# Kernel tuning notes

Hardware: AMD Instinct MI355X
Metric: run time of the kernel (lower is better)

Reference implementation:

```python
import jax, jax.numpy as jnp
import numpy as np

NUM_HEAD = 16
NUM_SEQ = 2048
NUM_FEAT = 1024
HEAD_DIM = NUM_FEAT // NUM_HEAD
LN_EPS = 1e-5


def _constants():
    # decay per head: log(1 - 2^{-5-h})
    decay = jnp.log(1.0 - 2.0 ** (-5.0 - jnp.arange(NUM_HEAD, dtype=jnp.float32)))
    idx = jnp.arange(NUM_SEQ, dtype=jnp.float32)
    diff = idx[:, None] - idx[None, :]                      # [s, s]
    # exp(diff * decay) on lower triangle (incl. diagonal), 0 above
    mask = jnp.where(diff[None] >= 0, jnp.exp(diff[None] * decay[:, None, None]), 0.0)  # [h, s, s]
    # rotary angles: each frequency repeated twice
    angle = 1.0 / 10000.0 ** jnp.linspace(0.0, 1.0, HEAD_DIM // 2)
    angle = jnp.repeat(angle, 2)                            # [hd]
    sin = jnp.sin(idx[:, None] * angle[None, :])            # [s, hd]
    cos = jnp.cos(idx[:, None] * angle[None, :])
    return mask, sin, cos


def _rotate_every_two(x):
    x1 = x[..., ::2]
    x2 = x[..., 1::2]
    return jnp.stack((-x2, x1), axis=-1).reshape(x.shape)


def setup_inputs() -> dict:
    key = jax.random.key(0)
    ks = jax.random.split(key, 5)
    b, s, d = 4, NUM_SEQ, NUM_FEAT
    x = jax.random.normal(ks[0], (b, s, d), dtype=jnp.float32)
    Wq = jax.random.normal(ks[1], (d, d), dtype=jnp.float32) * 0.02
    Wk = jax.random.normal(ks[2], (d, d), dtype=jnp.float32) * 0.02
    Wv = jax.random.normal(ks[3], (d, d), dtype=jnp.float32) * 0.02
    Wo = jax.random.normal(ks[4], (d, d), dtype=jnp.float32) * 0.02
    ln_w = jnp.ones((HEAD_DIM,), dtype=jnp.float32)
    ln_b = jnp.zeros((HEAD_DIM,), dtype=jnp.float32)
    return {"x": x, "Wq": Wq, "Wk": Wk, "Wv": Wv, "Wo": Wo, "ln_w": ln_w, "ln_b": ln_b}


def reference(x, Wq, Wk, Wv, Wo, ln_w, ln_b):
    b, s, d = x.shape
    h, hd = NUM_HEAD, HEAD_DIM
    mask, sin, cos = _constants()

    def proj(W):
        # torch Linear (no bias): x @ W.T -> [b, h, s, hd]
        return (x @ W.T).reshape(b, s, h, hd).transpose(0, 2, 1, 3)

    q, k, v = proj(Wq), proj(Wk), proj(Wv)
    # rotary theta shift (sin/cos broadcast over batch & head)
    q = q * cos + _rotate_every_two(q) * sin
    k = k * cos + _rotate_every_two(k) * sin

    r = jnp.einsum('bhsd,bhtd->bhst', q, k) * mask[None]    # decay-masked scores
    o = jnp.einsum('bhst,bhtd->bhsd', r, v)                 # [b, h, s, hd]

    # LayerNorm over head_dim
    mu = jnp.mean(o, axis=-1, keepdims=True)
    var = jnp.var(o, axis=-1, keepdims=True)
    y = (o - mu) * jax.lax.rsqrt(var + LN_EPS) * ln_w + ln_b

    y = y.transpose(0, 2, 1, 3).reshape(b, s, d)
    return jax.nn.silu(y) @ Wo.T
```

## Files before the change

### kernel.cpp

```cpp
#include <hip/hip_runtime.h>
#include <math.h>

typedef unsigned short u16;
typedef __attribute__((ext_vector_type(8))) short short8;
typedef __attribute__((ext_vector_type(4))) float floatx4;

#define LDS_AS(p) ((__attribute__((address_space(3))) void*)(p))
#define GLB_AS(p) ((const __attribute__((address_space(1))) void*)(p))

__device__ __forceinline__ u16 f2bf(float f) {
  unsigned int u = __float_as_uint(f);
  u += 0x7fffu + ((u >> 16) & 1u);
  return (u16)(u >> 16);
}

__device__ __forceinline__ void gld16(const void* g, void* l) {
  __builtin_amdgcn_global_load_lds(GLB_AS(g), LDS_AS(l), 16, 0, 0);
}

__device__ __forceinline__ floatx4 mfma16(short8 a, short8 b, floatx4 c) {
  return __builtin_amdgcn_mfma_f32_16x16x32_bf16(a, b, c, 0, 0, 0);
}

__global__ void prep_kernel(const float* __restrict__ x, const float* __restrict__ Wq,
                            const float* __restrict__ Wk, const float* __restrict__ Wv,
                            const float* __restrict__ Wo, u16* __restrict__ xp,
                            u16* __restrict__ wqkvp, u16* __restrict__ wop,
                            float2* __restrict__ rtab) {
  int i = blockIdx.x * blockDim.x + threadIdx.x;
  const int str = gridDim.x * blockDim.x;
  for (; i < 3211264; i += str) {
    if (i < 3145728) {
      int U; u16* d;
      const float* s;
      if (i < 2097152)      { U = i;           d = xp;    s = x;  }
      else if (i < 2883584) { U = i - 2097152; d = wqkvp; s = nullptr; }
      else                  { U = i - 2883584; d = wop;   s = Wo; }
      const int tile = U >> 12;
      const int kc   = (U >> 7) & 31;
      const int lane = (U >> 1) & 63;
      const int jh   = U & 1;
      const int scol = kc * 32 + (lane >> 4) * 8 + jh * 4;
      int srow = tile * 16 + (lane & 15);
      if (s == nullptr) {
        const int sel = srow >> 10;
        srow &= 1023;
        s = (sel == 0) ? Wq : (sel == 1) ? Wk : Wv;
      }
      float4 v = ((const float4*)s)[srow * 256 + (scol >> 2)];
      ushort4 o;
      o.x = f2bf(v.x); o.y = f2bf(v.y); o.z = f2bf(v.z); o.w = f2bf(v.w);
      ((ushort4*)d)[U] = o;
    } else {
      const int t = i - 3145728;
      const int seq = t >> 5, dh = t & 31;
      const float freq = exp2f(-(float)dh * 0.42863594770f);
      float sn, cs;
      __sincosf((float)seq * freq, &sn, &cs);
      rtab[t] = make_float2(sn, cs);
    }
  }
}

template <int EPI>
__global__ __launch_bounds__(512, 4)
void gemm_bt(const u16* __restrict__ A, const u16* __restrict__ Bw, int K,
             u16* __restrict__ qb, u16* __restrict__ kb, u16* __restrict__ vtb,
             u16* __restrict__ kwt, const float2* __restrict__ rtab,
             float* __restrict__ outp) {
  __shared__ __align__(16) u16 smem[36864];
  const int tid = threadIdx.x;
  const int w = tid >> 6, lane = tid & 63;
  const int quad = lane >> 4, l15 = lane & 15;
  const int wr = w >> 2, wc = w & 3;
  const int m0 = blockIdx.y * 128, n0 = blockIdx.x * 256;

  const size_t tsz = (size_t)(K >> 5) * 512;
  const u16* Apk = A + ((size_t)(m0 >> 4) + w) * tsz + lane * 8;
  const u16* B0  = Bw + ((size_t)(n0 >> 4) + 2 * w) * tsz + lane * 8;
  const u16* B1  = B0 + tsz;

  auto stage = [&](int buf, int kc) {
    const int nb = buf * 12288;
    gld16(Apk + (size_t)kc * 512, &smem[nb + w * 512]);
    gld16(B0 + (size_t)kc * 512, &smem[nb + 4096 + (2 * w) * 512]);
    gld16(B1 + (size_t)kc * 512, &smem[nb + 4096 + (2 * w + 1) * 512]);
  };

  floatx4 acc[4][4] = {};
  const int NT = K >> 5;

  stage(0, 0);
  stage(1, 1);

  int cur = 0, stg = 2;
  for (int t = 0; t < NT; ++t) {
    if (t + 1 < NT)
      asm volatile("s_waitcnt vmcnt(3)" ::: "memory");
    else
      asm volatile("s_waitcnt vmcnt(0)" ::: "memory");
    __builtin_amdgcn_s_barrier();
    asm volatile("" ::: "memory");
    __builtin_amdgcn_sched_barrier(0);

    if (t + 2 < NT) stage(stg, t + 2);

    const u16* Ap = &smem[cur * 12288];
    const u16* Bp = &smem[cur * 12288 + 4096];
    short8 a[4], b[4];
#pragma unroll
    for (int i = 0; i < 4; ++i)
      a[i] = *(const short8*)&Ap[(wr * 4 + i) * 512 + lane * 8];
#pragma unroll
    for (int j = 0; j < 4; ++j)
      b[j] = *(const short8*)&Bp[(wc * 4 + j) * 512 + lane * 8];
    __builtin_amdgcn_s_setprio(1);
#pragma unroll
    for (int i = 0; i < 4; ++i)
#pragma unroll
      for (int j = 0; j < 4; ++j)
        acc[i][j] = mfma16(a[i], b[j], acc[i][j]);
    __builtin_amdgcn_s_setprio(0);
    asm volatile("" ::: "memory");
    cur = (cur == 2) ? 0 : cur + 1;
    stg = (stg == 2) ? 0 : stg + 1;
  }
  __builtin_amdgcn_s_barrier();

  u16* scr = &smem[w * 4096];

  const int mrb = m0 + wr * 64;
  const int ncb = n0 + wc * 64;

  if (EPI == 0) {
    const int which = n0 >> 10;
    const int c1024 = ncb & 1023;
    const int bidx = mrb >> 11;
    const int hh = c1024 >> 6;
    const int seq0 = mrb & 2047;
    const int lr = lane >> 3, lc = lane & 7;

    if (which < 2) {
#pragma unroll
      for (int j = 0; j < 4; ++j) {
        const int d = j * 16 + l15;
        const int dc = d >> 3, dl = d & 7;
#pragma unroll
        for (int i = 0; i < 4; ++i)
#pragma unroll
          for (int r = 0; r < 4; ++r) {
            const int sl = i * 16 + quad * 4 + r;
            const int seq = seq0 + sl;
            const float v = acc[i][j][r];
            const float p = __shfl_xor(v, 1, 64);
            const float2 sc = rtab[(d >> 1) + seq * 32];
            const float res = (d & 1) ? (v * sc.y + p * sc.x) : (v * sc.y - p * sc.x);
            scr[sl * 64 + (((dc + (sl >> 2)) & 7) << 3) + dl] = f2bf(res);
          }
      }
      u16* dst = ((which == 0) ? qb : kb) + (size_t)(bidx * 16 + hh) * 131072 +
                 (size_t)seq0 * 64;
#pragma unroll
      for (int cch = 0; cch < 8; ++cch) {
        const int row = cch * 8 + lr;
        const int slot = (lc + (row >> 2)) & 7;
        short8 vv = *(const short8*)&scr[row * 64 + slot * 8];
        *(short8*)(dst + (size_t)row * 64 + lc * 8) = vv;
      }
      if (which == 1) {
        const float l2h = __log2f(1.0f - exp2f(-(float)(5 + hh)));
#pragma unroll
        for (int j = 0; j < 4; ++j) {
          const int d = j * 16 + l15;
#pragma unroll
          for (int i = 0; i < 4; ++i) {
            ushort4 pk;
#pragma unroll
            for (int r = 0; r < 4; ++r) {
              const int sl = i * 16 + quad * 4 + r;
              const int seq = seq0 + sl;
              const float v = acc[i][j][r];
              const float p = __shfl_xor(v, 1, 64);
              const float2 sc = rtab[(d >> 1) + seq * 32];
              const float res = (d & 1) ? (v * sc.y + p * sc.x) : (v * sc.y - p * sc.x);
              const float wgt = exp2f((float)(127 - (seq & 127)) * l2h);
              ((u16*)&pk)[r] = f2bf(res * wgt);
            }
            *(ushort4*)&scr[d * 64 + ((i * 16 + quad * 4 + 8 * (d & 7)) & 63)] = pk;
          }
        }
        u16* dw = kwt + (size_t)(bidx * 16 + hh) * 131072 + seq0;
#pragma unroll
        for (int cch = 0; cch < 8; ++cch) {
          const int drow = cch * 8 + lr;
          const int slot = (lc + (drow & 7)) & 7;
          short8 vv = *(const short8*)&scr[drow * 64 + slot * 8];
          *(short8*)(dw + (size_t)drow * 2048 + lc * 8) = vv;
        }
      }
    } else {
#pragma unroll
      for (int j = 0; j < 4; ++j) {
        const int d = j * 16 + l15;
#pragma unroll
        for (int i = 0; i < 4; ++i) {
          ushort4 pk;
          pk.x = f2bf(acc[i][j][0]);
          pk.y = f2bf(acc[i][j][1]);
          pk.z = f2bf(acc[i][j][2]);
          pk.w = f2bf(acc[i][j][3]);
          *(ushort4*)&scr[d * 64 + ((i * 16 + quad * 4 + 8 * (d & 7)) & 63)] = pk;
        }
      }
      u16* dh = vtb + (size_t)(bidx * 16 + hh) * 131072 + seq0;
#pragma unroll
      for (int cch = 0; cch < 8; ++cch) {
        const int drow = cch * 8 + lr;
        const int slot = (lc + (drow & 7)) & 7;
        short8 vv = *(const short8*)&scr[drow * 64 + slot * 8];
        *(short8*)(dh + (size_t)drow * 2048 + lc * 8) = vv;
      }
    }
  } else {
    float* scrf = (float*)scr;
    const int lr4 = lane >> 4, lc16 = lane & 15;
#pragma unroll
    for (int p = 0; p < 4; ++p) {
#pragma unroll
      for (int j = 0; j < 4; ++j)
#pragma unroll
        for (int r = 0; r < 4; ++r)
          scrf[(quad * 4 + r) * 65 + j * 16 + l15] = acc[p][j][r];
#pragma unroll
      for (int cch = 0; cch < 4; ++cch) {
        const int rr = cch * 4 + lr4;
        float4 vv = *(const float4*)&scrf[rr * 65 + lc16 * 4];
        *(float4*)&outp[(size_t)(mrb + p * 16 + rr) * 1024 + ncb + lc16 * 4] = vv;
      }
    }
  }
}

__global__ __launch_bounds__(256, 4)
void kvchunk_kernel(const u16* __restrict__ kwt, const u16* __restrict__ vtb,
                    float* __restrict__ U) {
  __shared__ __align__(16) u16 kls[16 * 512];
  __shared__ __align__(16) u16 vls[16 * 512];
  const int c = blockIdx.x, bh = blockIdx.y;
  const int tid = threadIdx.x, w = tid >> 6, lane = tid & 63;
  const int quad = lane >> 4, l15 = lane & 15;
  const u16* kg = kwt + (size_t)bh * 131072 + c * 128;
  const u16* vg = vtb + (size_t)bh * 131072 + c * 128;
#pragma unroll
  for (int rg = 0; rg < 4; ++rg) {
    const int rid = w * 4 + rg;
    const int m = rid >> 2, kst = rid & 3;
    gld16(kg + (size_t)(m * 16 + l15) * 2048 + kst * 32 + quad * 8, &kls[rid * 512]);
    gld16(vg + (size_t)(m * 16 + l15) * 2048 + kst * 32 + quad * 8, &vls[rid * 512]);
  }
  __syncthreads();
  floatx4 acc[4] = {};
#pragma unroll
  for (int kst = 0; kst < 4; ++kst) {
    short8 bf = *(const short8*)&vls[(w * 4 + kst) * 512 + lane * 8];
#pragma unroll
    for (int m = 0; m < 4; ++m) {
      short8 af = *(const short8*)&kls[(m * 4 + kst) * 512 + lane * 8];
      acc[m] = mfma16(af, bf, acc[m]);
    }
  }
  float* Ub = U + ((size_t)bh * 16 + c) * 4096;
#pragma unroll
  for (int m = 0; m < 4; ++m)
#pragma unroll
    for (int r = 0; r < 4; ++r)
      Ub[(m * 16 + quad * 4 + r) * 64 + w * 16 + l15] = acc[m][r];
}

__global__ void scan_kernel(const float* __restrict__ U, u16* __restrict__ Sb) {
  const int bh = blockIdx.x;
  const int w = threadIdx.x >> 6, l = threadIdx.x & 63;
  const int h = bh & 15;
  const float l2 = __log2f(1.0f - exp2f(-(float)(5 + h)));
  const float lamL = exp2f(128.0f * l2);
  float S[16];
#pragma unroll
  for (int i = 0; i < 16; ++i) S[i] = 0.f;
  for (int c = 0; c < 16; ++c) {
    u16* sp = Sb + ((size_t)bh * 16 + c) * 4096 + l * 64 + w * 16;
#pragma unroll
    for (int dk = 0; dk < 16; dk += 4) {
      ushort4 pk;
      pk.x = f2bf(S[dk]);     pk.y = f2bf(S[dk + 1]);
      pk.z = f2bf(S[dk + 2]); pk.w = f2bf(S[dk + 3]);
      *(ushort4*)&sp[dk] = pk;
    }
    const float* up = U + ((size_t)bh * 16 + c) * 4096 + (w * 16) * 64 + l;
#pragma unroll
    for (int dk = 0; dk < 16; ++dk)
      S[dk] = lamL * S[dk] + up[dk * 64];
  }
}

__global__ __launch_bounds__(256, 2)
void attn_chunk_kernel(const u16* __restrict__ qb, const u16* __restrict__ kb,
                       const u16* __restrict__ vtb, const u16* __restrict__ Sb,
                       const float* __restrict__ lnw, const float* __restrict__ lnb,
                       u16* __restrict__ yb) {
  __shared__ __align__(16) u16 kls[16 * 512];
  __shared__ __align__(16) u16 vls[16 * 512];
  __shared__ __align__(16) u16 Sls[8 * 512];
  __shared__ __align__(16) u16 pls[4 * 32 * 40];

  const int c = blockIdx.x, bh = blockIdx.y, h = bh & 15;
  const int tid = threadIdx.x;
  const int w = tid >> 6, lane = tid & 63, quad = lane >> 4, l15 = lane & 15;
  const float l2 = __log2f(1.0f - exp2f(-(float)(5 + h)));

  const u16* kg = kb + (size_t)bh * 131072 + (size_t)c * 128 * 64;
  const u16* vg = vtb + (size_t)bh * 131072 + (size_t)c * 128;
  const u16* Sg = Sb + ((size_t)bh * 16 + c) * 4096;
#pragma unroll
  for (int rg = 0; rg < 4; ++rg) {
    const int kid = w * 4 + rg;
    const int nsub = kid >> 1, kk = kid & 1;
    gld16(kg + (size_t)(nsub * 16 + l15) * 64 + kk * 32 + quad * 8, &kls[kid * 512]);
    const int jd = kid >> 2, kst = kid & 3;
    gld16(vg + (size_t)(jd * 16 + l15) * 2048 + kst * 32 + quad * 8, &vls[kid * 512]);
  }
#pragma unroll
  for (int e = 0; e < 2; ++e) {
    const int rid = w * 2 + e;
    const int nd = rid >> 1, kk = rid & 1;
    gld16(Sg + (size_t)(nd * 16 + l15) * 64 + kk * 32 + quad * 8, &Sls[rid * 512]);
  }

  short8 qf[2][2];
  {
    const u16* qbase = qb + ((size_t)bh * 2048 + c * 128 + w * 32 + l15) * 64 + quad * 8;
#pragma unroll
    for (int i = 0; i < 2; ++i)
#pragma unroll
      for (int kk = 0; kk < 2; ++kk)
        qf[i][kk] = *(const short8*)(qbase + (size_t)i * 16 * 64 + kk * 32);
  }
  float lnwv[4], lnbv[4];
#pragma unroll
  for (int jd = 0; jd < 4; ++jd) {
    lnwv[jd] = lnw[jd * 16 + l15];
    lnbv[jd] = lnb[jd * 16 + l15];
  }
  __syncthreads();

  floatx4 sacc[2][8] = {};
#pragma unroll
  for (int kk = 0; kk < 2; ++kk) {
    short8 bf[8];
#pragma unroll
    for (int j = 0; j < 8; ++j)
      bf[j] = *(const short8*)&kls[(j * 2 + kk) * 512 + lane * 8];
#pragma unroll
    for (int i = 0; i < 2; ++i)
#pragma unroll
      for (int j = 0; j < 8; ++j)
        sacc[i][j] = mfma16(qf[i][kk], bf[j], sacc[i][j]);
  }

  floatx4 oacc[2][4] = {};
#pragma unroll
  for (int kk = 0; kk < 2; ++kk)
#pragma unroll
    for (int nd = 0; nd < 4; ++nd) {
      short8 sf = *(const short8*)&Sls[(nd * 2 + kk) * 512 + lane * 8];
#pragma unroll
      for (int i = 0; i < 2; ++i)
        oacc[i][nd] = mfma16(qf[i][kk], sf, oacc[i][nd]);
    }
  float rowf[8];
#pragma unroll
  for (int i = 0; i < 2; ++i)
#pragma unroll
    for (int r = 0; r < 4; ++r)
      rowf[i * 4 + r] = exp2f((float)(w * 32 + i * 16 + quad * 4 + r) * l2);
  const float lam1 = exp2f(l2);
#pragma unroll
  for (int i = 0; i < 2; ++i)
#pragma unroll
    for (int nd = 0; nd < 4; ++nd)
#pragma unroll
      for (int r = 0; r < 4; ++r)
        oacc[i][nd][r] *= rowf[i * 4 + r] * lam1;

  float colf[8];
#pragma unroll
  for (int j = 0; j < 8; ++j) colf[j] = exp2f(-(float)(j * 16 + l15) * l2);
  u16* pw = &pls[w * 1280];
#pragma unroll
  for (int kst = 0; kst < 4; ++kst) {
#pragma unroll
    for (int jl = 0; jl < 2; ++jl) {
      const int j = kst * 2 + jl;
#pragma unroll
      for (int i = 0; i < 2; ++i)
#pragma unroll
        for (int r = 0; r < 4; ++r) {
          const int srow = i * 16 + quad * 4 + r;
          const int dlt = (w * 32 + srow) - (j * 16 + l15);
          const float v =
              (dlt >= 0) ? sacc[i][j][r] * rowf[i * 4 + r] * colf[j] : 0.0f;
          pw[srow * 40 + jl * 16 + l15] = f2bf(v);
        }
    }
    short8 pf[2], vf[4];
#pragma unroll
    for (int i = 0; i < 2; ++i)
      pf[i] = *(const short8*)&pw[(i * 16 + l15) * 40 + quad * 8];
#pragma unroll
    for (int jd = 0; jd < 4; ++jd)
      vf[jd] = *(const short8*)&vls[(jd * 4 + kst) * 512 + lane * 8];
#pragma unroll
    for (int i = 0; i < 2; ++i)
#pragma unroll
      for (int jd = 0; jd < 4; ++jd)
        oacc[i][jd] = mfma16(pf[i], vf[jd], oacc[i][jd]);
  }

  __syncthreads();
  u16* scrw = &kls[w * 2048];
  const int b = bh >> 4;
#pragma unroll
  for (int i = 0; i < 2; ++i)
#pragma unroll
    for (int r = 0; r < 4; ++r) {
      float sum = 0.f, ssq = 0.f;
#pragma unroll
      for (int jd = 0; jd < 4; ++jd) {
        const float v = oacc[i][jd][r];
        sum += v;
        ssq += v * v;
      }
#pragma unroll
      for (int off = 1; off < 16; off <<= 1) {
        sum += __shfl_xor(sum, off, 64);
        ssq += __shfl_xor(ssq, off, 64);
      }
      const float mu = sum * (1.0f / 64.0f);
      const float var = ssq * (1.0f / 64.0f) - mu * mu;
      const float rst = rsqrtf(var + 1e-5f);
      const int sl = i * 16 + quad * 4 + r;
#pragma unroll
      for (int jd = 0; jd < 4; ++jd) {
        const float z = (oacc[i][jd][r] - mu) * rst * lnwv[jd] + lnbv[jd];
        const float y = z / (1.0f + expf(-z));
        const int f = jd * 16 + l15;
        scrw[sl * 64 + ((((f >> 3) + (sl >> 2)) & 7) << 3) + (f & 7)] = f2bf(y);
      }
    }
  const int tile0 = b * 128 + c * 8 + w * 2;
#pragma unroll
  for (int tt = 0; tt < 2; ++tt)
#pragma unroll
    for (int kcl = 0; kcl < 2; ++kcl) {
      const int row = tt * 16 + l15;
      const int slot = ((kcl * 4 + quad) + (row >> 2)) & 7;
      short8 vv = *(const short8*)&scrw[row * 64 + slot * 8];
      *(short8*)(yb + ((size_t)(tile0 + tt) * 32 + h * 2 + kcl) * 512 + lane * 8) = vv;
    }
}

extern "C" void kernel_launch(void* const* d_in, const int* in_sizes, int n_in,
                              void* d_out, int out_size, void* d_ws, size_t ws_size,
                              hipStream_t stream) {
  const float* x   = (const float*)d_in[0];
  const float* Wq  = (const float*)d_in[1];
  const float* Wk  = (const float*)d_in[2];
  const float* Wv  = (const float*)d_in[3];
  const float* Wo  = (const float*)d_in[4];
  const float* lnw = (const float*)d_in[5];
  const float* lnb = (const float*)d_in[6];
  float* out = (float*)d_out;

  char* ws = (char*)d_ws;
  u16* xbf  = (u16*)(ws + 0);
  u16* wqkv = (u16*)(ws + 16777216);
  u16* Sb   = (u16*)(ws + 16777216);
  u16* qbuf = (u16*)(ws + 25165824);
  u16* kbuf = (u16*)(ws + 41943040);
  u16* vtb  = (u16*)(ws + 58720256);
  u16* wo   = (u16*)(ws + 75497472);
  float2* rtab = (float2*)(ws + 77594624);
  u16* yb   = xbf;
  u16* kwt  = (u16*)d_out;
  float* Ubuf = (float*)((char*)d_out + 16777216);

  prep_kernel<<<dim3(1024), dim3(256), 0, stream>>>(x, Wq, Wk, Wv, Wo, xbf, wqkv, wo,
                                                    rtab);
  gemm_bt<0><<<dim3(12, 64), dim3(512), 0, stream>>>(xbf, wqkv, 1024, qbuf, kbuf, vtb,
                                                     kwt, rtab, nullptr);
  kvchunk_kernel<<<dim3(16, 64), dim3(256), 0, stream>>>(kwt, vtb, Ubuf);
  scan_kernel<<<dim3(64), dim3(256), 0, stream>>>(Ubuf, Sb);
  attn_chunk_kernel<<<dim3(16, 64), dim3(256), 0, stream>>>(qbuf, kbuf, vtb, Sb, lnw,
                                                            lnb, yb);
  gemm_bt<1><<<dim3(4, 64), dim3(512), 0, stream>>>(yb, wo, 1024, nullptr, nullptr,
                                                    nullptr, nullptr, nullptr, out);
}
```

Before: 240.7 us.

## Enlarge GEMM block tile to 256x256 with four-stage LDS pipeline

```diff
diff --git a/kernel.cpp b/kernel.cpp
--- a/kernel.cpp
+++ b/kernel.cpp
@@ -63,179 +63,185 @@
 }
 
 template <int EPI>
-__global__ __launch_bounds__(512, 4)
+__global__ __launch_bounds__(512, 2)
 void gemm_bt(const u16* __restrict__ A, const u16* __restrict__ Bw, int K,
              u16* __restrict__ qb, u16* __restrict__ kb, u16* __restrict__ vtb,
              u16* __restrict__ kwt, const float2* __restrict__ rtab,
              float* __restrict__ outp) {
-  __shared__ __align__(16) u16 smem[36864];
+  __shared__ __align__(16) u16 smem[65536];
   const int tid = threadIdx.x;
   const int w = tid >> 6, lane = tid & 63;
   const int quad = lane >> 4, l15 = lane & 15;
   const int wr = w >> 2, wc = w & 3;
-  const int m0 = blockIdx.y * 128, n0 = blockIdx.x * 256;
+  const int m0 = blockIdx.y * 256, n0 = blockIdx.x * 256;
 
   const size_t tsz = (size_t)(K >> 5) * 512;
-  const u16* Apk = A + ((size_t)(m0 >> 4) + w) * tsz + lane * 8;
-  const u16* B0  = Bw + ((size_t)(n0 >> 4) + 2 * w) * tsz + lane * 8;
-  const u16* B1  = B0 + tsz;
+  const u16* A0 = A + ((size_t)(m0 >> 4) + 2 * w) * tsz + lane * 8;
+  const u16* A1 = A0 + tsz;
+  const u16* B0 = Bw + ((size_t)(n0 >> 4) + 2 * w) * tsz + lane * 8;
+  const u16* B1 = B0 + tsz;
 
   auto stage = [&](int buf, int kc) {
-    const int nb = buf * 12288;
-    gld16(Apk + (size_t)kc * 512, &smem[nb + w * 512]);
-    gld16(B0 + (size_t)kc * 512, &smem[nb + 4096 + (2 * w) * 512]);
-    gld16(B1 + (size_t)kc * 512, &smem[nb + 4096 + (2 * w + 1) * 512]);
+    const int nb = buf * 16384;
+    gld16(A0 + (size_t)kc * 512, &smem[nb + (2 * w) * 512]);
+    gld16(A1 + (size_t)kc * 512, &smem[nb + (2 * w + 1) * 512]);
+    gld16(B0 + (size_t)kc * 512, &smem[nb + 8192 + (2 * w) * 512]);
+    gld16(B1 + (size_t)kc * 512, &smem[nb + 8192 + (2 * w + 1) * 512]);
   };
 
-  floatx4 acc[4][4] = {};
+  floatx4 acc[8][4] = {};
   const int NT = K >> 5;
 
   stage(0, 0);
   stage(1, 1);
-
-  int cur = 0, stg = 2;
+  stage(2, 2);
+
   for (int t = 0; t < NT; ++t) {
-    if (t + 1 < NT)
-      asm volatile("s_waitcnt vmcnt(3)" ::: "memory");
+    if (t <= NT - 3)
+      asm volatile("s_waitcnt vmcnt(8)" ::: "memory");
+    else if (t == NT - 2)
+      asm volatile("s_waitcnt vmcnt(4)" ::: "memory");
     else
       asm volatile("s_waitcnt vmcnt(0)" ::: "memory");
     __builtin_amdgcn_s_barrier();
     asm volatile("" ::: "memory");
     __builtin_amdgcn_sched_barrier(0);
 
-    if (t + 2 < NT) stage(stg, t + 2);
-
-    const u16* Ap = &smem[cur * 12288];
-    const u16* Bp = &smem[cur * 12288 + 4096];
-    short8 a[4], b[4];
-#pragma unroll
-    for (int i = 0; i < 4; ++i)
-      a[i] = *(const short8*)&Ap[(wr * 4 + i) * 512 + lane * 8];
+    if (t + 3 < NT) stage((t + 3) & 3, t + 3);
+
+    const u16* Ap = &smem[(t & 3) * 16384];
+    const u16* Bp = Ap + 8192;
+    short8 a[8], b[4];
+#pragma unroll
+    for (int i = 0; i < 8; ++i)
+      a[i] = *(const short8*)&Ap[(wr * 8 + i) * 512 + lane * 8];
 #pragma unroll
     for (int j = 0; j < 4; ++j)
       b[j] = *(const short8*)&Bp[(wc * 4 + j) * 512 + lane * 8];
     __builtin_amdgcn_s_setprio(1);
 #pragma unroll
-    for (int i = 0; i < 4; ++i)
+    for (int i = 0; i < 8; ++i)
 #pragma unroll
       for (int j = 0; j < 4; ++j)
         acc[i][j] = mfma16(a[i], b[j], acc[i][j]);
     __builtin_amdgcn_s_setprio(0);
     asm volatile("" ::: "memory");
-    cur = (cur == 2) ? 0 : cur + 1;
-    stg = (stg == 2) ? 0 : stg + 1;
   }
   __builtin_amdgcn_s_barrier();
 
   u16* scr = &smem[w * 4096];
 
-  const int mrb = m0 + wr * 64;
   const int ncb = n0 + wc * 64;
-
-  if (EPI == 0) {
-    const int which = n0 >> 10;
-    const int c1024 = ncb & 1023;
-    const int bidx = mrb >> 11;
-    const int hh = c1024 >> 6;
-    const int seq0 = mrb & 2047;
-    const int lr = lane >> 3, lc = lane & 7;
-
-    if (which < 2) {
-#pragma unroll
-      for (int j = 0; j < 4; ++j) {
-        const int d = j * 16 + l15;
-        const int dc = d >> 3, dl = d & 7;
-#pragma unroll
-        for (int i = 0; i < 4; ++i)
-#pragma unroll
-          for (int r = 0; r < 4; ++r) {
-            const int sl = i * 16 + quad * 4 + r;
-            const int seq = seq0 + sl;
-            const float v = acc[i][j][r];
-            const float p = __shfl_xor(v, 1, 64);
-            const float2 sc = rtab[(d >> 1) + seq * 32];
-            const float res = (d & 1) ? (v * sc.y + p * sc.x) : (v * sc.y - p * sc.x);
-            scr[sl * 64 + (((dc + (sl >> 2)) & 7) << 3) + dl] = f2bf(res);
-          }
-      }
-      u16* dst = ((which == 0) ? qb : kb) + (size_t)(bidx * 16 + hh) * 131072 +
-                 (size_t)seq0 * 64;
-#pragma unroll
-      for (int cch = 0; cch < 8; ++cch) {
-        const int row = cch * 8 + lr;
-        const int slot = (lc + (row >> 2)) & 7;
-        short8 vv = *(const short8*)&scr[row * 64 + slot * 8];
-        *(short8*)(dst + (size_t)row * 64 + lc * 8) = vv;
-      }
-      if (which == 1) {
-        const float l2h = __log2f(1.0f - exp2f(-(float)(5 + hh)));
+  const int lr = lane >> 3, lc = lane & 7;
+
+#pragma unroll
+  for (int ih = 0; ih < 2; ++ih) {
+    const int mrb = m0 + wr * 128 + ih * 64;
+
+    if (EPI == 0) {
+      const int which = n0 >> 10;
+      const int c1024 = ncb & 1023;
+      const int bidx = mrb >> 11;
+      const int hh = c1024 >> 6;
+      const int seq0 = mrb & 2047;
+
+      if (which < 2) {
 #pragma unroll
         for (int j = 0; j < 4; ++j) {
           const int d = j * 16 + l15;
-#pragma unroll
-          for (int i = 0; i < 4; ++i) {
-            ushort4 pk;
+          const int dc = d >> 3, dl = d & 7;
+#pragma unroll
+          for (int i = 0; i < 4; ++i)
 #pragma unroll
             for (int r = 0; r < 4; ++r) {
               const int sl = i * 16 + quad * 4 + r;
               const int seq = seq0 + sl;
-              const float v = acc[i][j][r];
+              const float v = acc[ih * 4 + i][j][r];
               const float p = __shfl_xor(v, 1, 64);
               const float2 sc = rtab[(d >> 1) + seq * 32];
               const float res = (d & 1) ? (v * sc.y + p * sc.x) : (v * sc.y - p * sc.x);
-              const float wgt = exp2f((float)(127 - (seq & 127)) * l2h);
-              ((u16*)&pk)[r] = f2bf(res * wgt);
+              scr[sl * 64 + (((dc + (sl >> 2)) & 7) << 3) + dl] = f2bf(res);
             }
+        }
+        u16* dst = ((which == 0) ? qb : kb) + (size_t)(bidx * 16 + hh) * 131072 +
+                   (size_t)seq0 * 64;
+#pragma unroll
+        for (int cch = 0; cch < 8; ++cch) {
+          const int row = cch * 8 + lr;
+          const int slot = (lc + (row >> 2)) & 7;
+          short8 vv = *(const short8*)&scr[row * 64 + slot * 8];
+          *(short8*)(dst + (size_t)row * 64 + lc * 8) = vv;
+        }
+        if (which == 1) {
+          const float l2h = __log2f(1.0f - exp2f(-(float)(5 + hh)));
+#pragma unroll
+          for (int j = 0; j < 4; ++j) {
+            const int d = j * 16 + l15;
+#pragma unroll
+            for (int i = 0; i < 4; ++i) {
+              ushort4 pk;
+#pragma unroll
+              for (int r = 0; r < 4; ++r) {
+                const int sl = i * 16 + quad * 4 + r;
+                const int seq = seq0 + sl;
+                const float v = acc[ih * 4 + i][j][r];
+                const float p = __shfl_xor(v, 1, 64);
+                const float2 sc = rtab[(d >> 1) + seq * 32];
+                const float res = (d & 1) ? (v * sc.y + p * sc.x) : (v * sc.y - p * sc.x);
+                const float wgt = exp2f((float)(127 - (seq & 127)) * l2h);
+                ((u16*)&pk)[r] = f2bf(res * wgt);
+              }
+              *(ushort4*)&scr[d * 64 + ((i * 16 + quad * 4 + 8 * (d & 7)) & 63)] = pk;
+            }
+          }
+          u16* dw = kwt + (size_t)(bidx * 16 + hh) * 131072 + seq0;
+#pragma unroll
+          for (int cch = 0; cch < 8; ++cch) {
+            const int drow = cch * 8 + lr;
+            const int slot = (lc + (drow & 7)) & 7;
+            short8 vv = *(const short8*)&scr[drow * 64 + slot * 8];
+            *(short8*)(dw + (size_t)drow * 2048 + lc * 8) = vv;
+          }
+        }
+      } else {
+#pragma unroll
+        for (int j = 0; j < 4; ++j) {
+          const int d = j * 16 + l15;
+#pragma unroll
+          for (int i = 0; i < 4; ++i) {
+            ushort4 pk;
+            pk.x = f2bf(acc[ih * 4 + i][j][0]);
+            pk.y = f2bf(acc[ih * 4 + i][j][1]);
+            pk.z = f2bf(acc[ih * 4 + i][j][2]);
+            pk.w = f2bf(acc[ih * 4 + i][j][3]);
             *(ushort4*)&scr[d * 64 + ((i * 16 + quad * 4 + 8 * (d & 7)) & 63)] = pk;
           }
         }
-        u16* dw = kwt + (size_t)(bidx * 16 + hh) * 131072 + seq0;
+        u16* dh = vtb + (size_t)(bidx * 16 + hh) * 131072 + seq0;
 #pragma unroll
         for (int cch = 0; cch < 8; ++cch) {
           const int drow = cch * 8 + lr;
           const int slot = (lc + (drow & 7)) & 7;
           short8 vv = *(const short8*)&scr[drow * 64 + slot * 8];
-          *(short8*)(dw + (size_t)drow * 2048 + lc * 8) = vv;
+          *(short8*)(dh + (size_t)drow * 2048 + lc * 8) = vv;
         }
       }
     } else {
-#pragma unroll
-      for (int j = 0; j < 4; ++j) {
-        const int d = j * 16 + l15;
-#pragma unroll
-        for (int i = 0; i < 4; ++i) {
-          ushort4 pk;
-          pk.x = f2bf(acc[i][j][0]);
-          pk.y = f2bf(acc[i][j][1]);
-          pk.z = f2bf(acc[i][j][2]);
-          pk.w = f2bf(acc[i][j][3]);
-          *(ushort4*)&scr[d * 64 + ((i * 16 + quad * 4 + 8 * (d & 7)) & 63)] = pk;
-        }
-      }
-      u16* dh = vtb + (size_t)(bidx * 16 + hh) * 131072 + seq0;
-#pragma unroll
-      for (int cch = 0; cch < 8; ++cch) {
-        const int drow = cch * 8 + lr;
-        const int slot = (lc + (drow & 7)) & 7;
-        short8 vv = *(const short8*)&scr[drow * 64 + slot * 8];
-        *(short8*)(dh + (size_t)drow * 2048 + lc * 8) = vv;
-      }
-    }
-  } else {
-    float* scrf = (float*)scr;
-    const int lr4 = lane >> 4, lc16 = lane & 15;
-#pragma unroll
-    for (int p = 0; p < 4; ++p) {
-#pragma unroll
-      for (int j = 0; j < 4; ++j)
-#pragma unroll
-        for (int r = 0; r < 4; ++r)
-          scrf[(quad * 4 + r) * 65 + j * 16 + l15] = acc[p][j][r];
-#pragma unroll
-      for (int cch = 0; cch < 4; ++cch) {
-        const int rr = cch * 4 + lr4;
-        float4 vv = *(const float4*)&scrf[rr * 65 + lc16 * 4];
-        *(float4*)&outp[(size_t)(mrb + p * 16 + rr) * 1024 + ncb + lc16 * 4] = vv;
+      float* scrf = (float*)scr;
+      const int lr4 = lane >> 4, lc16 = lane & 15;
+#pragma unroll
+      for (int p = 0; p < 4; ++p) {
+#pragma unroll
+        for (int j = 0; j < 4; ++j)
+#pragma unroll
+          for (int r = 0; r < 4; ++r)
+            scrf[(quad * 4 + r) * 65 + j * 16 + l15] = acc[ih * 4 + p][j][r];
+#pragma unroll
+        for (int cch = 0; cch < 4; ++cch) {
+          const int rr = cch * 4 + lr4;
+          float4 vv = *(const float4*)&scrf[rr * 65 + lc16 * 4];
+          *(float4*)&outp[(size_t)(mrb + p * 16 + rr) * 1024 + ncb + lc16 * 4] = vv;
+        }
       }
     }
   }
@@ -495,12 +501,12 @@
 
   prep_kernel<<<dim3(1024), dim3(256), 0, stream>>>(x, Wq, Wk, Wv, Wo, xbf, wqkv, wo,
                                                     rtab);
-  gemm_bt<0><<<dim3(12, 64), dim3(512), 0, stream>>>(xbf, wqkv, 1024, qbuf, kbuf, vtb,
+  gemm_bt<0><<<dim3(12, 32), dim3(512), 0, stream>>>(xbf, wqkv, 1024, qbuf, kbuf, vtb,
                                                      kwt, rtab, nullptr);
   kvchunk_kernel<<<dim3(16, 64), dim3(256), 0, stream>>>(kwt, vtb, Ubuf);
   scan_kernel<<<dim3(64), dim3(256), 0, stream>>>(Ubuf, Sb);
   attn_chunk_kernel<<<dim3(16, 64), dim3(256), 0, stream>>>(qbuf, kbuf, vtb, Sb, lnw,
                                                             lnb, yb);
-  gemm_bt<1><<<dim3(4, 64), dim3(512), 0, stream>>>(yb, wo, 1024, nullptr, nullptr,
+  gemm_bt<1><<<dim3(4, 32), dim3(512), 0, stream>>>(yb, wo, 1024, nullptr, nullptr,
                                                     nullptr, nullptr, nullptr, out);
 }
```

Measured after the change: 266.4 us. 1.11x slower.
